# Kernel optimization log

Measured on AMD Instinct MI355X. Metric: run time of the kernel, lower is better.

The kernel has to match this reference:

```python
import jax, jax.numpy as jnp
import numpy as np

B, T, C = 4, 2048, 2048
N_HEAD, N_KV = 16, 4
HEAD_DIM = C // N_HEAD          # 128
KV_DIM = HEAD_DIM * N_KV        # 512
WINDOW = 256
ROPE_BASE = 10000.0


def setup_inputs() -> dict:
    key = jax.random.key(0)
    ks = jax.random.split(key, 5)
    s = 0.02
    return {
        "x": jax.random.normal(ks[0], (B, T, C), dtype=jnp.float32),
        "Wq": jax.random.normal(ks[1], (C, C), dtype=jnp.float32) * s,
        "Wk": jax.random.normal(ks[2], (C, KV_DIM), dtype=jnp.float32) * s,
        "Wv": jax.random.normal(ks[3], (C, KV_DIM), dtype=jnp.float32) * s,
        "Wo": jax.random.normal(ks[4], (C, C), dtype=jnp.float32) * s,
    }


def _rope(x):
    # x: [B, H, T, D]; GPT-NeoX half-split rotation
    d = x.shape[-1]
    t = x.shape[-2]
    inv_freq = 1.0 / (ROPE_BASE ** (jnp.arange(0, d, 2, dtype=jnp.float32) / d))
    freqs = jnp.arange(t, dtype=jnp.float32)[:, None] * inv_freq[None, :]  # [T, D/2]
    cos, sin = jnp.cos(freqs), jnp.sin(freqs)
    x1, x2 = x[..., : d // 2], x[..., d // 2:]
    return jnp.concatenate([x1 * cos - x2 * sin, x1 * sin + x2 * cos], axis=-1)


def reference(x, Wq, Wk, Wv, Wo):
    b, t, c = x.shape
    hd = HEAD_DIM
    q = (x @ Wq).reshape(b, t, N_HEAD, hd).transpose(0, 2, 1, 3)   # [B,nh,T,hd]
    k = (x @ Wk).reshape(b, t, N_KV, hd).transpose(0, 2, 1, 3)     # [B,nkv,T,hd]
    v = (x @ Wv).reshape(b, t, N_KV, hd).transpose(0, 2, 1, 3)

    q = _rope(q)
    k = _rope(k)

    # GQA: repeat kv heads to match query heads
    rep = N_HEAD // N_KV
    k = jnp.repeat(k, rep, axis=1)   # [B,nh,T,hd]
    v = jnp.repeat(v, rep, axis=1)

    att = jnp.einsum("bhqd,bhkd->bhqk", q, k) / jnp.sqrt(jnp.float32(hd))
    i = jnp.arange(t)[:, None]
    j = jnp.arange(t)[None, :]
    # causal AND sliding window: i - WINDOW <= j <= i
    mask = (j <= i) & (j >= i - WINDOW)
    att = jnp.where(mask[None, None], att, jnp.finfo(att.dtype).min)
    att = jax.nn.softmax(att, axis=-1)

    y = jnp.einsum("bhqk,bhkd->bhqd", att, v)          # [B,nh,T,hd]
    y = y.transpose(0, 2, 1, 3).reshape(b, t, c)       # [B,T,C]
    return y @ Wo
```

## Files before the change

kernel.cpp:

```cpp
#include <hip/hip_runtime.h>
#include <stdint.h>

#define T_ 2048
#define C_ 2048
#define HD 128
#define LDQKV 3072

typedef unsigned short u16;
typedef __attribute__((ext_vector_type(8))) short bf16x8;
typedef __attribute__((ext_vector_type(4))) float f32x4;
typedef __attribute__((ext_vector_type(4))) float float4v;
typedef __attribute__((ext_vector_type(4))) u16 u16x4;
typedef __attribute__((ext_vector_type(8))) u16 u16x8;

typedef __attribute__((address_space(3))) void lds_void;
typedef const __attribute__((address_space(1))) void gbl_void;

__device__ __forceinline__ void gload_lds16(const void* g, void* l) {
  __builtin_amdgcn_global_load_lds((gbl_void*)(uintptr_t)g,
                                   (lds_void*)(uint32_t)(uintptr_t)l, 16, 0, 0);
}

__device__ __forceinline__ u16 f2bf(float f) {
  union { float f; uint32_t u; } v; v.f = f;
  uint32_t r = v.u + 0x7FFFu + ((v.u >> 16) & 1u);
  return (u16)(r >> 16);
}
__device__ __forceinline__ float bf2f(u16 h) {
  union { uint32_t u; float f; } v; v.u = ((uint32_t)h) << 16;
  return v.f;
}

#define BAR() do { asm volatile("" ::: "memory"); __builtin_amdgcn_s_barrier(); asm volatile("" ::: "memory"); } while (0)
#define VMCNT(n) asm volatile("s_waitcnt vmcnt(" #n ")" ::: "memory")
template<int N> __device__ __forceinline__ void VMCNT_C() {
  if constexpr (N == 0) { VMCNT(0); }
  else if constexpr (N == 3) { VMCNT(3); }
  else if constexpr (N == 4) { VMCNT(4); }
  else { static_assert(N == 0 || N == 3 || N == 4, "add literal"); }
}

__device__ __forceinline__ void ttile(const float* __restrict__ src, int ldw, int nb,
                                      int k0, int n0out, u16* __restrict__ out, int tid,
                                      float (*Lt)[68]) {
  int kr = tid >> 4, nc = (tid & 15) * 4;
#pragma unroll
  for (int s = 0; s < 4; ++s) {
    float4v v = *(const float4v*)(src + (size_t)(k0 + kr + 16 * s) * ldw + nb + nc);
#pragma unroll
    for (int e = 0; e < 4; ++e) Lt[kr + 16 * s][nc + e] = v[e];
  }
  __syncthreads();
  int nr = tid & 31, kc = (tid >> 5) * 8;
#pragma unroll
  for (int s2 = 0; s2 < 2; ++s2) {
    int n = nr + 32 * s2;
    u16x8 o;
#pragma unroll
    for (int e = 0; e < 8; ++e) o[e] = f2bf(Lt[kc + e][n]);
    *(u16x8*)(out + (size_t)(n0out + n) * 2048 + k0 + kc) = o;
  }
}

__global__ __launch_bounds__(256) void k_prep(const float* __restrict__ x,
                                              const float* __restrict__ Wq, const float* __restrict__ Wk,
                                              const float* __restrict__ Wv, const float* __restrict__ Wo,
                                              u16* __restrict__ xbf, u16* __restrict__ wtq,
                                              u16* __restrict__ wot, float* __restrict__ cst) {
  __shared__ float Lt[64][68];
  const int bid = blockIdx.x, tid = threadIdx.x;
  if (bid < 16384) {
    size_t idx = (size_t)bid * 256 + tid;
    float4v xv = *(const float4v*)(x + idx * 4);
    u16x4 r;
#pragma unroll
    for (int e = 0; e < 4; ++e) r[e] = f2bf(xv[e]);
    *(u16x4*)(xbf + idx * 4) = r;
  } else if (bid < 17920) {
    int b = bid - 16384;
    int n0 = (b % 48) * 64, k0 = (b / 48) * 64;
    const float* src; int ldw, nb;
    if (n0 < 2048)      { src = Wq; ldw = 2048; nb = n0; }
    else if (n0 < 2560) { src = Wk; ldw = 512;  nb = n0 - 2048; }
    else                { src = Wv; ldw = 512;  nb = n0 - 2560; }
    ttile(src, ldw, nb, k0, n0, wtq, tid, Lt);
  } else if (bid < 18944) {
    int b = bid - 17920;
    ttile(Wo, 2048, (b % 32) * 64, (b / 32) * 64, (b % 32) * 64, wot, tid, Lt);
  } else {
    int idx = (bid - 18944) * 256 + tid;
    int t = idx >> 6, d = idx & 63;
    float inv = expf(-(float)d * (1.0f / 64.0f) * 9.2103403719761836f);
    float f = (float)t * inv;
    float s, c;
    sincosf(f, &s, &c);
    cst[idx * 2] = c;
    cst[idx * 2 + 1] = s;
  }
}

__global__ __launch_bounds__(256) void k_rope(u16* __restrict__ qkv, const float* __restrict__ cst) {
  int idx = blockIdx.x * 256 + threadIdx.x;
  int token = idx / 160;
  int rem = idx - token * 160;
  int hd = rem >> 3, oct = rem & 7;
  int col = ((hd < 16) ? hd * 128 : 2048 + (hd - 16) * 128) + oct * 8;
  size_t base = (size_t)token * LDQKV + col;
  int t = token & (T_ - 1);
  float sc = (hd < 16) ? 0.08838834764831845f : 1.0f;
  u16x8 a = *(const u16x8*)(qkv + base);
  u16x8 b2 = *(const u16x8*)(qkv + base + 64);
  const float* cp = cst + (size_t)(t * 64 + oct * 8) * 2;
  u16x8 ra, rb;
#pragma unroll
  for (int e = 0; e < 8; ++e) {
    float c = cp[e * 2], s = cp[e * 2 + 1];
    float x1 = bf2f(a[e]), x2 = bf2f(b2[e]);
    ra[e] = f2bf((x1 * c - x2 * s) * sc);
    rb[e] = f2bf((x1 * s + x2 * c) * sc);
  }
  *(u16x8*)(qkv + base) = ra;
  *(u16x8*)(qkv + base + 64) = rb;
}

template<int OUTF32, int NF>
__global__ __launch_bounds__(512, 1) void k_gemm8(const u16* __restrict__ A, const u16* __restrict__ Bt,
                                                  void* __restrict__ Cout, int M, int N, int K, int nbx) {
  constexpr int BUFE = 16384 + NF * 4096;
  __shared__ __attribute__((aligned(16))) u16 lds[2 * BUFE];
  const int tid = threadIdx.x, lane = tid & 63;
  const int w = tid >> 6, wm = w >> 2, wn = w & 3;
  const int l15 = lane & 15, lhi = lane >> 4;
  const int nwg = gridDim.x, cpx = nwg >> 3;
  const int wg = (blockIdx.x & 7) * cpx + (blockIdx.x >> 3);
  const int bx = wg % nbx, by = wg / nbx;
  const int m0 = by * 256, n0 = bx * (NF * 64);
  const int NT = K >> 6;

  const int srow = tid >> 3;
  const int scol = ((tid & 7) ^ (srow & 7)) * 8;
  const u16* pA0 = A + (size_t)(m0 + srow) * K + scol;
  const u16* pA1 = pA0 + (size_t)64 * K;
  const u16* pA2 = pA0 + (size_t)128 * K;
  const u16* pA3 = pA0 + (size_t)192 * K;
  const u16* pB0 = Bt + (size_t)(n0 + srow) * K + scol;
  const u16* pB1 = pB0 + (size_t)64 * K;
  const u16* pB2 = pB0 + (size_t)128 * K;
  const u16* pB3 = pB0 + (size_t)(NF == 4 ? 192 : 128) * K;
  u16* dEA = lds + tid * 8;
  u16* dEB = lds + 16384 + tid * 8;
  u16* dOA = lds + BUFE + tid * 8;
  u16* dOB = lds + BUFE + 16384 + tid * 8;
  const int xk0 = (lhi ^ (l15 & 7)) * 8;
  const int xk1 = ((4 + lhi) ^ (l15 & 7)) * 8;
  const u16* rAe0 = lds + (wm * 128 + l15) * 64 + xk0;
  const u16* rAe1 = lds + (wm * 128 + l15) * 64 + xk1;
  const u16* rBe0 = lds + 16384 + (wn * (NF * 16) + l15) * 64 + xk0;
  const u16* rBe1 = lds + 16384 + (wn * (NF * 16) + l15) * 64 + xk1;
  const u16* rAo0 = rAe0 + BUFE;
  const u16* rAo1 = rAe1 + BUFE;
  const u16* rBo0 = rBe0 + BUFE;
  const u16* rBo1 = rBe1 + BUFE;

  f32x4 acc[8][NF];
#pragma unroll
  for (int i = 0; i < 8; ++i)
#pragma unroll
    for (int j = 0; j < NF; ++j) acc[i][j] = (f32x4){0.f, 0.f, 0.f, 0.f};

  gload_lds16(pA0, dEA);         gload_lds16(pA1, dEA + 4096);
  gload_lds16(pA2, dEA + 8192);  gload_lds16(pA3, dEA + 12288);
  gload_lds16(pB0, dEB);         gload_lds16(pB1, dEB + 4096);
  gload_lds16(pB2, dEB + 8192);
  if constexpr (NF == 4) gload_lds16(pB3, dEB + 12288);
  pB0 += 64; pB1 += 64; pB2 += 64;
  if constexpr (NF == 4) pB3 += 64;
  gload_lds16(pB0, dOB);         gload_lds16(pB1, dOB + 4096);
  gload_lds16(pB2, dOB + 8192);
  if constexpr (NF == 4) gload_lds16(pB3, dOB + 12288);
  VMCNT_C<NF>();
  BAR();

  auto TILE = [&](const u16* rA0, const u16* rA1, const u16* rB0, const u16* rB1,
                  u16* dA, u16* dB, bool stA, bool nlast) {
    bf16x8 bb[NF][2], aa[4][2];
    auto MH = [&](int h) {
#pragma unroll
      for (int ks = 0; ks < 2; ++ks)
#pragma unroll
        for (int mi = 0; mi < 4; ++mi)
#pragma unroll
          for (int nf = 0; nf < NF; ++nf)
            acc[h * 4 + mi][nf] = __builtin_amdgcn_mfma_f32_16x16x32_bf16(
                aa[mi][ks], bb[nf][ks], acc[h * 4 + mi][nf], 0, 0, 0);
    };
#pragma unroll
    for (int nf = 0; nf < NF; ++nf) {
      bb[nf][0] = *(const bf16x8*)(rB0 + nf * 1024);
      bb[nf][1] = *(const bf16x8*)(rB1 + nf * 1024);
    }
#pragma unroll
    for (int mi = 0; mi < 4; ++mi) {
      aa[mi][0] = *(const bf16x8*)(rA0 + mi * 1024);
      aa[mi][1] = *(const bf16x8*)(rA1 + mi * 1024);
    }
    if (stA) {
      pA0 += 64; pA1 += 64; pA2 += 64; pA3 += 64;
      gload_lds16(pA0, dA);        gload_lds16(pA1, dA + 4096);
      gload_lds16(pA2, dA + 8192); gload_lds16(pA3, dA + 12288);
    }
    __builtin_amdgcn_s_setprio(1);
    MH(0);
    __builtin_amdgcn_s_setprio(0);
    BAR();
#pragma unroll
    for (int mi = 0; mi < 4; ++mi) {
      aa[mi][0] = *(const bf16x8*)(rA0 + 4096 + mi * 1024);
      aa[mi][1] = *(const bf16x8*)(rA1 + 4096 + mi * 1024);
    }
    if (nlast) {
      pB0 += 64; pB1 += 64; pB2 += 64;
      gload_lds16(pB0, dB);        gload_lds16(pB1, dB + 4096);
      gload_lds16(pB2, dB + 8192);
      if constexpr (NF == 4) { pB3 += 64; gload_lds16(pB3, dB + 12288); }
    }
    __builtin_amdgcn_s_setprio(1);
    MH(1);
    __builtin_amdgcn_s_setprio(0);
    if (nlast) { VMCNT_C<NF>(); } else { VMCNT_C<0>(); }
    BAR();
  };

  for (int t = 0; t < NT; t += 2) {
    const bool nlast = (t + 2 < NT);
    TILE(rAe0, rAe1, rBe0, rBe1, dOA, dEB, true,  nlast);
    TILE(rAo0, rAo1, rBo0, rBo1, dEA, dOB, nlast, nlast);
  }

#pragma unroll
  for (int mf = 0; mf < 8; ++mf) {
#pragma unroll
    for (int nf = 0; nf < NF; ++nf) {
      int col = n0 + wn * (NF * 16) + nf * 16 + l15;
#pragma unroll
      for (int r = 0; r < 4; ++r) {
        int row = m0 + wm * 128 + mf * 16 + lhi * 4 + r;
        float v = acc[mf][nf][r];
        if (OUTF32) ((float*)Cout)[(size_t)row * N + col] = v;
        else        ((u16*)Cout)[(size_t)row * N + col] = f2bf(v);
      }
    }
  }
}

__global__ __launch_bounds__(256) void k_attn(const u16* __restrict__ qkv, u16* __restrict__ y) {
  const int bid = blockIdx.x;
  const int qt = bid & 31, h = (bid >> 5) & 15, b = bid >> 9;
  const int i0 = qt * 64;
  const size_t tb = (size_t)b * T_ * LDQKV;
  const u16* qb = qkv + tb + h * HD;
  const u16* kb = qkv + tb + 2048 + (h >> 2) * HD;
  const u16* vb = kb + 512;
  __shared__ __attribute__((aligned(16))) u16 smem[20480];
  u16* Ks = smem;
  u16* Vt = smem + 8192;
  u16* Psw = smem + 16384;
  u16* Qs = smem;
  const int tid = threadIdx.x, lane = tid & 63, w = tid >> 6;
  const int l15 = lane & 15, lhi = lane >> 4;
  u16* Ps = Psw + w * 1024;

#pragma unroll
  for (int it = 0; it < 4; ++it) {
    int c = it * 256 + tid, row = c >> 4, kc = (c & 15) ^ (row & 7);
    gload_lds16(qb + (size_t)(i0 + row) * LDQKV + kc * 8, &Qs[(it * 256 + w * 64) * 8]);
  }
  __syncthreads();
  bf16x8 qf[4];
#pragma unroll
  for (int ks = 0; ks < 4; ++ks) {
    int row = w * 16 + l15;
    int kc = (ks * 4 + lhi) ^ (row & 7);
    qf[ks] = *(const bf16x8*)&Qs[(row * 16 + kc) * 8];
  }
  __syncthreads();

  f32x4 o[8];
#pragma unroll
  for (int dt = 0; dt < 8; ++dt) o[dt] = (f32x4){0.f, 0.f, 0.f, 0.f};
  float mrun[4], lrun[4];
#pragma unroll
  for (int r = 0; r < 4; ++r) { mrun[r] = -1e30f; lrun[r] = 0.f; }

  const int jb0 = (i0 >= 256) ? (i0 - 256) : 0;
  for (int jb = jb0; jb <= i0; jb += 64) {
#pragma unroll
    for (int it = 0; it < 4; ++it) {
      int c = it * 256 + tid, row = c >> 4, kc = (c & 15) ^ (row & 7);
      gload_lds16(kb + (size_t)(jb + row) * LDQKV + kc * 8, &Ks[(it * 256 + w * 64) * 8]);
    }
#pragma unroll
    for (int it = 0; it < 4; ++it) {
      int chunk = it * 256 + tid, row = chunk >> 4, dc = chunk & 15;
      u16x8 vv = *(const u16x8*)(vb + (size_t)(jb + row) * LDQKV + dc * 8);
#pragma unroll
      for (int e = 0; e < 8; ++e) {
        int d = dc * 8 + e;
        int s = (dc ^ e) & 7;
        Vt[d * 64 + (row ^ (s << 3))] = vv[e];
      }
    }
    __syncthreads();

    f32x4 s[4];
#pragma unroll
    for (int t = 0; t < 4; ++t) {
      s[t] = (f32x4){0.f, 0.f, 0.f, 0.f};
#pragma unroll
      for (int ks = 0; ks < 4; ++ks) {
        int row = t * 16 + l15;
        int kc = (ks * 4 + lhi) ^ (row & 7);
        bf16x8 kf = *(const bf16x8*)&Ks[(row * 16 + kc) * 8];
        s[t] = __builtin_amdgcn_mfma_f32_16x16x32_bf16(qf[ks], kf, s[t], 0, 0, 0);
      }
    }

    const int irow0 = i0 + w * 16 + lhi * 4;
    float rmax[4];
#pragma unroll
    for (int r = 0; r < 4; ++r) rmax[r] = -1e30f;
#pragma unroll
    for (int t = 0; t < 4; ++t) {
      int j = jb + t * 16 + l15;
#pragma unroll
      for (int r = 0; r < 4; ++r) {
        int i = irow0 + r;
        float sv = s[t][r];
        sv = (j <= i && j + 256 >= i) ? sv : -1e30f;
        s[t][r] = sv;
        rmax[r] = fmaxf(rmax[r], sv);
      }
    }
#pragma unroll
    for (int r = 0; r < 4; ++r) {
#pragma unroll
      for (int off = 1; off < 16; off <<= 1)
        rmax[r] = fmaxf(rmax[r], __shfl_xor(rmax[r], off));
    }
    float sf[4], psum[4];
#pragma unroll
    for (int r = 0; r < 4; ++r) {
      float mn = fmaxf(mrun[r], rmax[r]);
      sf[r] = __expf(mrun[r] - mn);
      mrun[r] = mn;
      psum[r] = 0.f;
    }
#pragma unroll
    for (int t = 0; t < 4; ++t) {
#pragma unroll
      for (int r = 0; r < 4; ++r) {
        float p = __expf(s[t][r] - mrun[r]);
        psum[r] += p;
        int q = lhi * 4 + r;
        int k = t * 16 + l15;
        Ps[q * 64 + (k ^ ((q & 7) << 3))] = f2bf(p);
      }
    }
#pragma unroll
    for (int r = 0; r < 4; ++r) {
#pragma unroll
      for (int off = 1; off < 16; off <<= 1)
        psum[r] += __shfl_xor(psum[r], off);
      lrun[r] = lrun[r] * sf[r] + psum[r];
    }
#pragma unroll
    for (int dt = 0; dt < 8; ++dt)
#pragma unroll
      for (int r = 0; r < 4; ++r)
        o[dt][r] = o[dt][r] * sf[r];

    bf16x8 pf[2];
#pragma unroll
    for (int ks2 = 0; ks2 < 2; ++ks2)
      pf[ks2] = *(const bf16x8*)&Ps[l15 * 64 + ((ks2 * 32 + lhi * 8) ^ ((l15 & 7) << 3))];
#pragma unroll
    for (int dt = 0; dt < 8; ++dt) {
#pragma unroll
      for (int ks2 = 0; ks2 < 2; ++ks2) {
        int d = dt * 16 + l15;
        int s2 = ((d >> 3) ^ (d & 7)) & 7;
        bf16x8 vf = *(const bf16x8*)&Vt[d * 64 + ((ks2 * 32 + lhi * 8) ^ (s2 << 3))];
        o[dt] = __builtin_amdgcn_mfma_f32_16x16x32_bf16(pf[ks2], vf, o[dt], 0, 0, 0);
      }
    }
    __syncthreads();
  }

#pragma unroll
  for (int dt = 0; dt < 8; ++dt) {
#pragma unroll
    for (int r = 0; r < 4; ++r) {
      int i = i0 + w * 16 + lhi * 4 + r;
      float v = o[dt][r] / lrun[r];
      y[((size_t)b * T_ + i) * C_ + h * HD + dt * 16 + l15] = f2bf(v);
    }
  }
}

extern "C" void kernel_launch(void* const* d_in, const int* in_sizes, int n_in,
                              void* d_out, int out_size, void* d_ws, size_t ws_size,
                              hipStream_t stream) {
  const float* x  = (const float*)d_in[0];
  const float* Wq = (const float*)d_in[1];
  const float* Wk = (const float*)d_in[2];
  const float* Wv = (const float*)d_in[3];
  const float* Wo = (const float*)d_in[4];
  char* ws = (char*)d_ws;
  u16* x_bf   = (u16*)(ws);
  u16* wt_qkv = (u16*)(ws + 33554432);
  u16* wo_t   = (u16*)(ws + 46137344);
  u16* qkv    = (u16*)(ws + 54525952);
  float* cst  = (float*)(ws + 104857600);
  u16* ybuf = x_bf;

  k_prep<<<19456, 256, 0, stream>>>(x, Wq, Wk, Wv, Wo, x_bf, wt_qkv, wo_t, cst);

  k_gemm8<0, 3><<<512, 512, 0, stream>>>(x_bf, wt_qkv, (void*)qkv, 8192, 3072, 2048, 16);

  k_rope<<<5120, 256, 0, stream>>>(qkv, cst);
  k_attn<<<2048, 256, 0, stream>>>(qkv, ybuf);

  k_gemm8<1, 4><<<256, 512, 0, stream>>>(ybuf, wo_t, d_out, 8192, 2048, 2048, 8);
}
```

Before: 286.5 us.

## Double-buffer K tiles and prefetch V into registers in sliding-window attention

The attention loop now keeps two LDS buffers for K, so the next tile's K is loaded asynchronously while the current tile is computed. The next tile's V rows are prefetched into registers and transposed into LDS at the start of the following iteration, using paired 2-element stores instead of scalar stores. MFMA sections are wrapped in s_setprio hints, and __syncthreads is replaced by raw barriers with explicit lgkmcnt waits. This costs more LDS and registers per block, which may lower occupancy, and correctness depends on implicit vmcnt ordering.

Measured after the change: 284.1 us. About the same (-0.8%).

```diff
diff --git a/kernel.cpp b/kernel.cpp
--- a/kernel.cpp
+++ b/kernel.cpp
@@ -12,6 +12,7 @@
 typedef __attribute__((ext_vector_type(4))) float float4v;
 typedef __attribute__((ext_vector_type(4))) u16 u16x4;
 typedef __attribute__((ext_vector_type(8))) u16 u16x8;
+typedef __attribute__((ext_vector_type(2))) u16 u16x2;
 
 typedef __attribute__((address_space(3))) void lds_void;
 typedef const __attribute__((address_space(1))) void gbl_void;
@@ -33,6 +34,7 @@
 
 #define BAR() do { asm volatile("" ::: "memory"); __builtin_amdgcn_s_barrier(); asm volatile("" ::: "memory"); } while (0)
 #define VMCNT(n) asm volatile("s_waitcnt vmcnt(" #n ")" ::: "memory")
+#define LGKM0()  asm volatile("s_waitcnt lgkmcnt(0)" ::: "memory")
 template<int N> __device__ __forceinline__ void VMCNT_C() {
   if constexpr (N == 0) { VMCNT(0); }
   else if constexpr (N == 3) { VMCNT(3); }
@@ -261,11 +263,12 @@
   const u16* qb = qkv + tb + h * HD;
   const u16* kb = qkv + tb + 2048 + (h >> 2) * HD;
   const u16* vb = kb + 512;
-  __shared__ __attribute__((aligned(16))) u16 smem[20480];
-  u16* Ks = smem;
-  u16* Vt = smem + 8192;
-  u16* Psw = smem + 16384;
-  u16* Qs = smem;
+  __shared__ __attribute__((aligned(16))) u16 smem[28672];
+  u16* KsA = smem;
+  u16* KsB = smem + 8192;
+  u16* Vt  = smem + 16384;
+  u16* Psw = smem + 24576;
+  u16* Qs  = smem;
   const int tid = threadIdx.x, lane = tid & 63, w = tid >> 6;
   const int l15 = lane & 15, lhi = lane >> 4;
   u16* Ps = Psw + w * 1024;
@@ -273,7 +276,7 @@
 #pragma unroll
   for (int it = 0; it < 4; ++it) {
     int c = it * 256 + tid, row = c >> 4, kc = (c & 15) ^ (row & 7);
-    gload_lds16(qb + (size_t)(i0 + row) * LDQKV + kc * 8, &Qs[(it * 256 + w * 64) * 8]);
+    gload_lds16(qb + (size_t)(i0 + row) * LDQKV + kc * 8, &Qs[c * 8]);
   }
   __syncthreads();
   bf16x8 qf[4];
@@ -293,26 +296,57 @@
   for (int r = 0; r < 4; ++r) { mrun[r] = -1e30f; lrun[r] = 0.f; }
 
   const int jb0 = (i0 >= 256) ? (i0 - 256) : 0;
-  for (int jb = jb0; jb <= i0; jb += 64) {
-#pragma unroll
-    for (int it = 0; it < 4; ++it) {
-      int c = it * 256 + tid, row = c >> 4, kc = (c & 15) ^ (row & 7);
-      gload_lds16(kb + (size_t)(jb + row) * LDQKV + kc * 8, &Ks[(it * 256 + w * 64) * 8]);
-    }
-#pragma unroll
-    for (int it = 0; it < 4; ++it) {
-      int chunk = it * 256 + tid, row = chunk >> 4, dc = chunk & 15;
-      u16x8 vv = *(const u16x8*)(vb + (size_t)(jb + row) * LDQKV + dc * 8);
-#pragma unroll
-      for (int e = 0; e < 8; ++e) {
-        int d = dc * 8 + e;
-        int s = (dc ^ e) & 7;
-        Vt[d * 64 + (row ^ (s << 3))] = vv[e];
-      }
-    }
-    __syncthreads();
+  const int ntile = ((i0 - jb0) >> 6) + 1;
+
+  const int vrow = (tid >> 4) << 1;
+  const int vdc  = tid & 15;
+#pragma unroll
+  for (int it = 0; it < 4; ++it) {
+    int c = it * 256 + tid, row = c >> 4, kc = (c & 15) ^ (row & 7);
+    gload_lds16(kb + (size_t)(jb0 + row) * LDQKV + kc * 8, &KsA[c * 8]);
+  }
+  u16x8 vA0, vA1, vB0, vB1;
+  {
+    const u16* vp = vb + (size_t)(jb0 + vrow) * LDQKV + vdc * 8;
+    vA0 = *(const u16x8*)vp;
+    vA1 = *(const u16x8*)(vp + LDQKV);
+    const u16* vp2 = vp + (size_t)32 * LDQKV;
+    vB0 = *(const u16x8*)vp2;
+    vB1 = *(const u16x8*)(vp2 + LDQKV);
+  }
+
+  for (int tau = 0; tau < ntile; ++tau) {
+    const int jb = jb0 + tau * 64;
+    const u16* Kc = (tau & 1) ? KsB : KsA;
+    u16* Kn = (tau & 1) ? KsA : KsB;
+#pragma unroll
+    for (int e = 0; e < 8; ++e) {
+      int d = vdc * 8 + e;
+      int s = (vdc ^ e) & 7;
+      u16x2 p0; p0[0] = vA0[e]; p0[1] = vA1[e];
+      *(u16x2*)&Vt[d * 64 + (vrow ^ (s << 3))] = p0;
+      u16x2 p1; p1[0] = vB0[e]; p1[1] = vB1[e];
+      *(u16x2*)&Vt[d * 64 + ((vrow + 32) ^ (s << 3))] = p1;
+    }
+    if (tau + 1 < ntile) {
+      const int jn = jb + 64;
+#pragma unroll
+      for (int it = 0; it < 4; ++it) {
+        int c = it * 256 + tid, row = c >> 4, kc = (c & 15) ^ (row & 7);
+        gload_lds16(kb + (size_t)(jn + row) * LDQKV + kc * 8, &Kn[c * 8]);
+      }
+      const u16* vp = vb + (size_t)(jn + vrow) * LDQKV + vdc * 8;
+      vA0 = *(const u16x8*)vp;
+      vA1 = *(const u16x8*)(vp + LDQKV);
+      const u16* vp2 = vp + (size_t)32 * LDQKV;
+      vB0 = *(const u16x8*)vp2;
+      vB1 = *(const u16x8*)(vp2 + LDQKV);
+    }
+    LGKM0();
+    BAR();
 
     f32x4 s[4];
+    __builtin_amdgcn_s_setprio(1);
 #pragma unroll
     for (int t = 0; t < 4; ++t) {
       s[t] = (f32x4){0.f, 0.f, 0.f, 0.f};
@@ -320,10 +354,11 @@
       for (int ks = 0; ks < 4; ++ks) {
         int row = t * 16 + l15;
         int kc = (ks * 4 + lhi) ^ (row & 7);
-        bf16x8 kf = *(const bf16x8*)&Ks[(row * 16 + kc) * 8];
+        bf16x8 kf = *(const bf16x8*)&Kc[(row * 16 + kc) * 8];
         s[t] = __builtin_amdgcn_mfma_f32_16x16x32_bf16(qf[ks], kf, s[t], 0, 0, 0);
       }
     }
+    __builtin_amdgcn_s_setprio(0);
 
     const int irow0 = i0 + w * 16 + lhi * 4;
     float rmax[4];
@@ -383,6 +418,7 @@
 #pragma unroll
     for (int ks2 = 0; ks2 < 2; ++ks2)
       pf[ks2] = *(const bf16x8*)&Ps[l15 * 64 + ((ks2 * 32 + lhi * 8) ^ ((l15 & 7) << 3))];
+    __builtin_amdgcn_s_setprio(1);
 #pragma unroll
     for (int dt = 0; dt < 8; ++dt) {
 #pragma unroll
@@ -393,7 +429,8 @@
         o[dt] = __builtin_amdgcn_mfma_f32_16x16x32_bf16(pf[ks2], vf, o[dt], 0, 0, 0);
       }
     }
-    __syncthreads();
+    __builtin_amdgcn_s_setprio(0);
+    BAR();
   }
 
 #pragma unroll
```
